# Performance work log

Measured on AMD Instinct MI355X. Metric: run time of the kernel, lower is better.

## Reference

```python
import jax, jax.numpy as jnp
import numpy as np

# DREAMPlace IDXST_IDCT (a.k.a. idsct2): y[u,v] = sum_p sum_q x[p,q] * sin(pi*p*(u+0.5)/M) * cos(pi*q*(v+0.5)/N)
# i.e. IDXST (inverse discrete sine transform, DST-III-like, unnormalized) along the M axis
# and IDCT (DCT-III-like, unnormalized, full weight on k=0) along the N axis.
# Computed with the classic 2N-padded FFT trick using the precomputed twiddles
# expk[k] = exp(-1j*pi*k/(2N)) stored as [N,2] (real, imag), matching precompute_expk.

def _idxt_spectrum(x, expk):
    """F[u] = sum_k x[k] * exp(-1j*pi*k*(2u+1)/(2N)), along last axis.
    Re(F) is the IDCT sum (cos), -Im(F) is the IDXST sum (sin)."""
    N = x.shape[-1]
    c = (x * expk[..., 0]) + 1j * (x * expk[..., 1])  # x[k] * exp(-j*pi*k/(2N))
    z = jnp.concatenate([c, jnp.zeros_like(c)], axis=-1)  # zero-pad to 2N
    return jnp.fft.fft(z, axis=-1)[..., :N]


def idct_1d(x, expk):
    # y[u] = sum_k x[k] cos(pi*k*(2u+1)/(2N))
    return _idxt_spectrum(x, expk).real


def idxst_1d(x, expk):
    # y[u] = sum_k x[k] sin(pi*k*(2u+1)/(2N))
    return -_idxt_spectrum(x, expk).imag


def _make_expk(L):
    k = jnp.arange(L, dtype=jnp.float32) * (np.pi / (2.0 * L))
    return jnp.stack([jnp.cos(k), -jnp.sin(k)], axis=-1)  # exp(-j*pi*k/(2L))


def setup_inputs() -> dict:
    M, N = 4096, 4096
    key = jax.random.key(0)
    x = jax.random.normal(key, (M, N), dtype=jnp.float32)
    return {"x": x, "expkM": _make_expk(M), "expkN": _make_expk(N)}


def reference(x, expkM, expkN):
    # IDCT along the last dim (N), then IDXST along the second-to-last dim (M):
    # idxst(idct(x)^T)^T
    t = idct_1d(x, expkN)                                        # [M, N]
    y = idxst_1d(t.swapaxes(-2, -1), expkM).swapaxes(-2, -1)     # [M, N]
    return y
```

## Files before the change

### kernel.cpp

```cpp
#include <hip/hip_runtime.h>
#include <hip/hip_bf16.h>
#include <stdint.h>
#include <cmath>


typedef __attribute__((ext_vector_type(4))) float f32x4;
typedef __attribute__((ext_vector_type(8))) unsigned short u16x8;
typedef __attribute__((ext_vector_type(8))) __bf16 bf16x8;

__device__ __forceinline__ unsigned short f2bf(float f) {
  union { float f; unsigned u; } v; v.f = f;
  unsigned u = v.u + 0x7fffu + ((v.u >> 16) & 1u);
  return (unsigned short)(u >> 16);
}
__device__ __forceinline__ float bf2f(unsigned short h) {
  union { unsigned u; float f; } v; v.u = ((unsigned)h) << 16;
  return v.f;
}

__device__ __forceinline__ void gen_half(int idx, u16x8* Pe, u16x8* Po,
                                         int isSin, int jshift, int jmask,
                                         unsigned mask4L, float sc) {
  int i = idx >> jshift;
  int jb = (idx & jmask) * 8;
  unsigned tp = 2u * (unsigned)i + 1u;
  unsigned re = (2u * (unsigned)jb * tp) & mask4L;
  unsigned ro = (re + tp) & mask4L;
  unsigned step = (2u * tp) & mask4L;
  u16x8 pe, po;
#pragma unroll
  for (int t = 0; t < 8; t++) {
    float se_, ce_, so_, co_;
    __sincosf((float)re * sc, &se_, &ce_);
    __sincosf((float)ro * sc, &so_, &co_);
    pe[t] = f2bf(isSin ? se_ : ce_);
    po[t] = f2bf(isSin ? so_ : co_);
    re = (re + step) & mask4L;
    ro = (ro + step) & mask4L;
  }
  Pe[idx] = pe;
  Po[idx] = po;
}

__global__ void prep_kernel(const f32x4* __restrict__ x, u16x8* __restrict__ xe,
                            u16x8* __restrict__ xo, u16x8* __restrict__ Ce,
                            u16x8* __restrict__ Co, u16x8* __restrict__ Se,
                            u16x8* __restrict__ So, int nConvBlocks,
                            int nGenNBlocks, int jshiftN, int jmaskN,
                            unsigned mask4N, float scN, int jshiftM, int jmaskM,
                            unsigned mask4M, float scM) {
  int b = blockIdx.x;
  if (b < nConvBlocks) {
    int idx = b * 256 + threadIdx.x;
    f32x4 a = x[4 * idx], bb = x[4 * idx + 1], c = x[4 * idx + 2],
          d = x[4 * idx + 3];
    u16x8 e, o;
    e[0] = f2bf(a[0]);  o[0] = f2bf(a[1]);  e[1] = f2bf(a[2]);  o[1] = f2bf(a[3]);
    e[2] = f2bf(bb[0]); o[2] = f2bf(bb[1]); e[3] = f2bf(bb[2]); o[3] = f2bf(bb[3]);
    e[4] = f2bf(c[0]);  o[4] = f2bf(c[1]);  e[5] = f2bf(c[2]);  o[5] = f2bf(c[3]);
    e[6] = f2bf(d[0]);  o[6] = f2bf(d[1]);  e[7] = f2bf(d[2]);  o[7] = f2bf(d[3]);
    xe[idx] = e;
    xo[idx] = o;
  } else if (b < nConvBlocks + nGenNBlocks) {
    int idx = (b - nConvBlocks) * 256 + threadIdx.x;
    gen_half(idx, Ce, Co, 0, jshiftN, jmaskN, mask4N, scN);
  } else {
    int idx = (b - nConvBlocks - nGenNBlocks) * 256 + threadIdx.x;
    gen_half(idx, Se, So, 1, jshiftM, jmaskM, mask4M, scM);
  }
}

__global__ __launch_bounds__(256, 2) void btgemm_kernel(
    const unsigned short* __restrict__ A0,
    const unsigned short* __restrict__ A1,
    const unsigned short* __restrict__ B0,
    const unsigned short* __restrict__ B1,
    unsigned short* __restrict__ C0, unsigned short* __restrict__ C1, int Ndim,
    int K) {
  __shared__ unsigned short As[128 * 64];
  __shared__ unsigned short Bs[128 * 64];

  const unsigned short* A = blockIdx.z ? A1 : A0;
  const unsigned short* Bt = blockIdx.z ? B1 : B0;
  unsigned short* C = blockIdx.z ? C1 : C0;

  const int tid = threadIdx.x;
  const int m0 = blockIdx.y * 128;
  const int n0 = blockIdx.x * 128;

  const int wave = tid >> 6;
  const int lane = tid & 63;
  const int wm = (wave & 1) * 64;
  const int wn = (wave >> 1) * 64;
  const int l16 = lane & 15;
  const int quad = lane >> 4;

  f32x4 acc[4][4];
#pragma unroll
  for (int i = 0; i < 4; i++)
#pragma unroll
    for (int j = 0; j < 4; j++) acc[i][j] = f32x4{0.f, 0.f, 0.f, 0.f};

  const int lrow = lane >> 3;
  const int lsw = ((lane & 7) ^ lrow) * 8;
  const unsigned short* Ag[4];
  const unsigned short* Bg[4];
  unsigned short* Al[4];
  unsigned short* Bl[4];
#pragma unroll
  for (int t = 0; t < 4; t++) {
    int ch = wave + 4 * t;
    Ag[t] = A + (size_t)(m0 + 8 * ch + lrow) * K + lsw;
    Bg[t] = Bt + (size_t)(n0 + 8 * ch + lrow) * K + lsw;
    Al[t] = As + ch * 512;
    Bl[t] = Bs + ch * 512;
  }

  const int swz = (quad ^ (l16 & 7)) * 8;

  for (int k0 = 0; k0 < K; k0 += 64) {
#pragma unroll
    for (int t = 0; t < 4; t++) {
      __builtin_amdgcn_global_load_lds(
          (const __attribute__((address_space(1))) void*)(Ag[t] + k0),
          (__attribute__((address_space(3))) void*)Al[t], 16, 0, 0);
      __builtin_amdgcn_global_load_lds(
          (const __attribute__((address_space(1))) void*)(Bg[t] + k0),
          (__attribute__((address_space(3))) void*)Bl[t], 16, 0, 0);
    }
    __syncthreads();

#pragma unroll
    for (int h = 0; h < 2; h++) {
      const int so = swz ^ (h * 32);
      bf16x8 af[4], bfr[4];
#pragma unroll
      for (int i = 0; i < 4; i++) {
        af[i]  = *(const bf16x8*)(As + (wm + i * 16 + l16) * 64 + so);
        bfr[i] = *(const bf16x8*)(Bs + (wn + i * 16 + l16) * 64 + so);
      }
#pragma unroll
      for (int i = 0; i < 4; i++)
#pragma unroll
        for (int j = 0; j < 4; j++)
          acc[i][j] = __builtin_amdgcn_mfma_f32_16x16x32_bf16(
              af[i], bfr[j], acc[i][j], 0, 0, 0);
    }
    __syncthreads();
  }

#pragma unroll
  for (int i = 0; i < 4; i++) {
#pragma unroll
    for (int j = 0; j < 4; j++) {
      int col = n0 + wn + j * 16 + l16;
      int rowb = m0 + wm + i * 16 + quad * 4;
#pragma unroll
      for (int r = 0; r < 4; r++)
        C[(size_t)(rowb + r) * Ndim + col] = f2bf(acc[i][j][r]);
    }
  }
}

__global__ void bfly1_kernel(const u16x8* __restrict__ E1,
                             const u16x8* __restrict__ O1,
                             u16x8* __restrict__ tTe, u16x8* __restrict__ tTo,
                             int pshift, int pmask, int Nrows, int Mh8) {
  int idx = blockIdx.x * blockDim.x + threadIdx.x;
  int v = idx >> pshift;
  int pu = idx & pmask;
  u16x8 e0 = E1[2 * idx], e1 = E1[2 * idx + 1];
  u16x8 o0 = O1[2 * idx], o1 = O1[2 * idx + 1];
  u16x8 tet, tot, teb, tob;
#pragma unroll
  for (int k = 0; k < 4; k++) {
    float ee = bf2f(e0[2 * k]), eo = bf2f(e0[2 * k + 1]);
    float oe = bf2f(o0[2 * k]), oo = bf2f(o0[2 * k + 1]);
    tet[k] = f2bf(ee + oe); tot[k] = f2bf(eo + oo);
    teb[k] = f2bf(ee - oe); tob[k] = f2bf(eo - oo);
  }
#pragma unroll
  for (int k = 0; k < 4; k++) {
    float ee = bf2f(e1[2 * k]), eo = bf2f(e1[2 * k + 1]);
    float oe = bf2f(o1[2 * k]), oo = bf2f(o1[2 * k + 1]);
    tet[4 + k] = f2bf(ee + oe); tot[4 + k] = f2bf(eo + oo);
    teb[4 + k] = f2bf(ee - oe); tob[4 + k] = f2bf(eo - oo);
  }
  tTe[idx] = tet;
  tTo[idx] = tot;
  int idxb = (Nrows - 1 - v) * Mh8 + pu;
  tTe[idxb] = teb;
  tTo[idxb] = tob;
}

__global__ void bfly2_kernel(const u16x8* __restrict__ E2,
                             const u16x8* __restrict__ O2,
                             f32x4* __restrict__ y, int vshift, int vmask,
                             int Mrows, int N4) {
  int idx = blockIdx.x * blockDim.x + threadIdx.x;
  int u = idx >> vshift;
  int vu = (idx & vmask) * 4;
  u16x8 e0 = E2[2 * idx], e1 = E2[2 * idx + 1];
  u16x8 o0 = O2[2 * idx], o1 = O2[2 * idx + 1];
  int baset = u * N4 + vu;
  int baseb = (Mrows - 1 - u) * N4 + vu;
#pragma unroll
  for (int t = 0; t < 2; t++) {
    f32x4 tv, bv;
#pragma unroll
    for (int k = 0; k < 4; k++) {
      float e = bf2f(e0[t * 4 + k]);
      float o = bf2f(o0[t * 4 + k]);
      tv[k] = e + o;
      bv[k] = o - e;
    }
    y[baset + t] = tv;
    y[baseb + t] = bv;
  }
#pragma unroll
  for (int t = 0; t < 2; t++) {
    f32x4 tv, bv;
#pragma unroll
    for (int k = 0; k < 4; k++) {
      float e = bf2f(e1[t * 4 + k]);
      float o = bf2f(o1[t * 4 + k]);
      tv[k] = e + o;
      bv[k] = o - e;
    }
    y[baset + 2 + t] = tv;
    y[baseb + 2 + t] = bv;
  }
}

extern "C" void kernel_launch(void* const* d_in, const int* in_sizes, int n_in,
                              void* d_out, int out_size, void* d_ws,
                              size_t ws_size, hipStream_t stream) {
  const float* x = (const float*)d_in[0];
  const int M = in_sizes[1] / 2;
  const int N = in_sizes[2] / 2;
  const size_t MN = (size_t)M * N;

  unsigned short* ws = (unsigned short*)d_ws;
  unsigned short* xe = ws;
  unsigned short* xo = ws + MN / 2;
  unsigned short* Ce = ws + MN;
  unsigned short* Co = ws + MN + MN / 4;
  unsigned short* Se = ws + MN * 3 / 2;
  unsigned short* So = ws + MN * 7 / 4;
  unsigned short* E1 = ws + MN * 2;
  unsigned short* O1 = ws + MN * 5 / 2;
  unsigned short* tTe = ws + MN * 3;
  unsigned short* tTo = ws + MN * 7 / 2;
  unsigned short* E2 = xe;
  unsigned short* O2 = xo;

  int shiftN = 0; while ((1 << shiftN) < N) shiftN++;
  int shiftM = 0; while ((1 << shiftM) < M) shiftM++;

  int nConvBlocks = (int)(MN / 16 / 256);
  int nGenNBlocks = (N / 2) * (N / 2) / 8 / 256;
  int nGenMBlocks = (M / 2) * (M / 2) / 8 / 256;
  prep_kernel<<<nConvBlocks + nGenNBlocks + nGenMBlocks, 256, 0, stream>>>(
      (const f32x4*)x, (u16x8*)xe, (u16x8*)xo, (u16x8*)Ce, (u16x8*)Co,
      (u16x8*)Se, (u16x8*)So, nConvBlocks, nGenNBlocks, shiftN - 4,
      (N / 16) - 1, (unsigned)(4 * N - 1),
      (float)(3.14159265358979323846 / (2.0 * N)), shiftM - 4, (M / 16) - 1,
      (unsigned)(4 * M - 1), (float)(3.14159265358979323846 / (2.0 * M)));

  btgemm_kernel<<<dim3(M / 128, (N / 2) / 128, 2), 256, 0, stream>>>(
      Ce, Co, xe, xo, E1, O1, M, N / 2);

  bfly1_kernel<<<(int)(MN / 32 / 256), 256, 0, stream>>>(
      (const u16x8*)E1, (const u16x8*)O1, (u16x8*)tTe, (u16x8*)tTo, shiftM - 4,
      (M / 16) - 1, N, M / 16);

  btgemm_kernel<<<dim3(N / 128, (M / 2) / 128, 2), 256, 0, stream>>>(
      Se, So, tTe, tTo, E2, O2, N, M / 2);

  bfly2_kernel<<<(int)(MN / 32 / 256), 256, 0, stream>>>(
      (const u16x8*)E2, (const u16x8*)O2, (f32x4*)d_out, shiftN - 4,
      (N / 16) - 1, M, N / 4);
}
```

Measured before the change: 282.3 us.

## Fuse butterfly stages into GEMM epilogues, computing even and odd products per block

Each GEMM block now computes both the even and odd partial products sequentially into two accumulator sets, then applies the butterfly (sum/difference with mirrored row) directly in the epilogue, writing either the transposed bf16 intermediate or the final fp32 output. This removes the two standalone butterfly kernels and the E/O intermediate round trips through global memory. In exchange each block does twice the K-loop work with half the grid (no z dimension), doubles accumulator registers (risking occupancy at 2 blocks/SM), and epilogue stores become scattered 2-byte/4-byte writes with strided columns.

```diff
diff --git a/kernel.cpp b/kernel.cpp
--- a/kernel.cpp
+++ b/kernel.cpp
@@ -12,10 +12,6 @@
   union { float f; unsigned u; } v; v.f = f;
   unsigned u = v.u + 0x7fffu + ((v.u >> 16) & 1u);
   return (unsigned short)(u >> 16);
-}
-__device__ __forceinline__ float bf2f(unsigned short h) {
-  union { unsigned u; float f; } v; v.u = ((unsigned)h) << 16;
-  return v.f;
 }
 
 __device__ __forceinline__ void gen_half(int idx, u16x8* Pe, u16x8* Po,
@@ -70,19 +66,16 @@
   }
 }
 
-__global__ __launch_bounds__(256, 2) void btgemm_kernel(
-    const unsigned short* __restrict__ A0,
-    const unsigned short* __restrict__ A1,
-    const unsigned short* __restrict__ B0,
-    const unsigned short* __restrict__ B1,
-    unsigned short* __restrict__ C0, unsigned short* __restrict__ C1, int Ndim,
-    int K) {
+template <int STAGE>
+__global__ __launch_bounds__(256, 2) void fused_gemm_kernel(
+    const unsigned short* __restrict__ Ae,
+    const unsigned short* __restrict__ Ao,
+    const unsigned short* __restrict__ Be,
+    const unsigned short* __restrict__ Bo,
+    unsigned short* __restrict__ out0, unsigned short* __restrict__ out1,
+    int outStride, int K, int Lfull) {
   __shared__ unsigned short As[128 * 64];
   __shared__ unsigned short Bs[128 * 64];
-
-  const unsigned short* A = blockIdx.z ? A1 : A0;
-  const unsigned short* Bt = blockIdx.z ? B1 : B0;
-  unsigned short* C = blockIdx.z ? C1 : C0;
 
   const int tid = threadIdx.x;
   const int m0 = blockIdx.y * 128;
@@ -95,140 +88,95 @@
   const int l16 = lane & 15;
   const int quad = lane >> 4;
 
-  f32x4 acc[4][4];
-#pragma unroll
-  for (int i = 0; i < 4; i++)
-#pragma unroll
-    for (int j = 0; j < 4; j++) acc[i][j] = f32x4{0.f, 0.f, 0.f, 0.f};
-
   const int lrow = lane >> 3;
   const int lsw = ((lane & 7) ^ lrow) * 8;
-  const unsigned short* Ag[4];
-  const unsigned short* Bg[4];
   unsigned short* Al[4];
   unsigned short* Bl[4];
 #pragma unroll
   for (int t = 0; t < 4; t++) {
     int ch = wave + 4 * t;
-    Ag[t] = A + (size_t)(m0 + 8 * ch + lrow) * K + lsw;
-    Bg[t] = Bt + (size_t)(n0 + 8 * ch + lrow) * K + lsw;
     Al[t] = As + ch * 512;
     Bl[t] = Bs + ch * 512;
   }
-
   const int swz = (quad ^ (l16 & 7)) * 8;
 
-  for (int k0 = 0; k0 < K; k0 += 64) {
+  f32x4 accE[4][4], accO[4][4];
+
+  auto kloop = [&](const unsigned short* __restrict__ A,
+                   const unsigned short* __restrict__ Bt,
+                   f32x4 (&acc)[4][4]) {
+#pragma unroll
+    for (int i = 0; i < 4; i++)
+#pragma unroll
+      for (int j = 0; j < 4; j++) acc[i][j] = f32x4{0.f, 0.f, 0.f, 0.f};
+
+    const unsigned short* Ag[4];
+    const unsigned short* Bg[4];
 #pragma unroll
     for (int t = 0; t < 4; t++) {
-      __builtin_amdgcn_global_load_lds(
-          (const __attribute__((address_space(1))) void*)(Ag[t] + k0),
-          (__attribute__((address_space(3))) void*)Al[t], 16, 0, 0);
-      __builtin_amdgcn_global_load_lds(
-          (const __attribute__((address_space(1))) void*)(Bg[t] + k0),
-          (__attribute__((address_space(3))) void*)Bl[t], 16, 0, 0);
+      int ch = wave + 4 * t;
+      Ag[t] = A + (size_t)(m0 + 8 * ch + lrow) * K + lsw;
+      Bg[t] = Bt + (size_t)(n0 + 8 * ch + lrow) * K + lsw;
     }
-    __syncthreads();
-
-#pragma unroll
-    for (int h = 0; h < 2; h++) {
-      const int so = swz ^ (h * 32);
-      bf16x8 af[4], bfr[4];
-#pragma unroll
-      for (int i = 0; i < 4; i++) {
-        af[i]  = *(const bf16x8*)(As + (wm + i * 16 + l16) * 64 + so);
-        bfr[i] = *(const bf16x8*)(Bs + (wn + i * 16 + l16) * 64 + so);
+
+    for (int k0 = 0; k0 < K; k0 += 64) {
+#pragma unroll
+      for (int t = 0; t < 4; t++) {
+        __builtin_amdgcn_global_load_lds(
+            (const __attribute__((address_space(1))) void*)(Ag[t] + k0),
+            (__attribute__((address_space(3))) void*)Al[t], 16, 0, 0);
+        __builtin_amdgcn_global_load_lds(
+            (const __attribute__((address_space(1))) void*)(Bg[t] + k0),
+            (__attribute__((address_space(3))) void*)Bl[t], 16, 0, 0);
       }
-#pragma unroll
-      for (int i = 0; i < 4; i++)
-#pragma unroll
-        for (int j = 0; j < 4; j++)
-          acc[i][j] = __builtin_amdgcn_mfma_f32_16x16x32_bf16(
-              af[i], bfr[j], acc[i][j], 0, 0, 0);
+      __syncthreads();
+
+#pragma unroll
+      for (int h = 0; h < 2; h++) {
+        const int so = swz ^ (h * 32);
+        bf16x8 af[4], bfr[4];
+#pragma unroll
+        for (int i = 0; i < 4; i++) {
+          af[i]  = *(const bf16x8*)(As + (wm + i * 16 + l16) * 64 + so);
+          bfr[i] = *(const bf16x8*)(Bs + (wn + i * 16 + l16) * 64 + so);
+        }
+#pragma unroll
+        for (int i = 0; i < 4; i++)
+#pragma unroll
+          for (int j = 0; j < 4; j++)
+            acc[i][j] = __builtin_amdgcn_mfma_f32_16x16x32_bf16(
+                af[i], bfr[j], acc[i][j], 0, 0, 0);
+      }
+      __syncthreads();
     }
-    __syncthreads();
-  }
+  };
+
+  kloop(Ae, Be, accE);
+  kloop(Ao, Bo, accO);
 
 #pragma unroll
   for (int i = 0; i < 4; i++) {
 #pragma unroll
     for (int j = 0; j < 4; j++) {
-      int col = n0 + wn + j * 16 + l16;
-      int rowb = m0 + wm + i * 16 + quad * 4;
-#pragma unroll
-      for (int r = 0; r < 4; r++)
-        C[(size_t)(rowb + r) * Ndim + col] = f2bf(acc[i][j][r]);
+      int n = n0 + wn + j * 16 + l16;
+      int mb = m0 + wm + i * 16 + quad * 4;
+#pragma unroll
+      for (int r = 0; r < 4; r++) {
+        float e = accE[i][j][r];
+        float o = accO[i][j][r];
+        int m = mb + r;
+        if (STAGE == 1) {
+          unsigned short* mat = (n & 1) ? out1 : out0;
+          int c = n >> 1;
+          mat[(size_t)m * outStride + c] = f2bf(e + o);
+          mat[(size_t)(Lfull - 1 - m) * outStride + c] = f2bf(e - o);
+        } else {
+          float* y = (float*)out0;
+          y[(size_t)m * outStride + n] = e + o;
+          y[(size_t)(Lfull - 1 - m) * outStride + n] = o - e;
+        }
+      }
     }
-  }
-}
-
-__global__ void bfly1_kernel(const u16x8* __restrict__ E1,
-                             const u16x8* __restrict__ O1,
-                             u16x8* __restrict__ tTe, u16x8* __restrict__ tTo,
-                             int pshift, int pmask, int Nrows, int Mh8) {
-  int idx = blockIdx.x * blockDim.x + threadIdx.x;
-  int v = idx >> pshift;
-  int pu = idx & pmask;
-  u16x8 e0 = E1[2 * idx], e1 = E1[2 * idx + 1];
-  u16x8 o0 = O1[2 * idx], o1 = O1[2 * idx + 1];
-  u16x8 tet, tot, teb, tob;
-#pragma unroll
-  for (int k = 0; k < 4; k++) {
-    float ee = bf2f(e0[2 * k]), eo = bf2f(e0[2 * k + 1]);
-    float oe = bf2f(o0[2 * k]), oo = bf2f(o0[2 * k + 1]);
-    tet[k] = f2bf(ee + oe); tot[k] = f2bf(eo + oo);
-    teb[k] = f2bf(ee - oe); tob[k] = f2bf(eo - oo);
-  }
-#pragma unroll
-  for (int k = 0; k < 4; k++) {
-    float ee = bf2f(e1[2 * k]), eo = bf2f(e1[2 * k + 1]);
-    float oe = bf2f(o1[2 * k]), oo = bf2f(o1[2 * k + 1]);
-    tet[4 + k] = f2bf(ee + oe); tot[4 + k] = f2bf(eo + oo);
-    teb[4 + k] = f2bf(ee - oe); tob[4 + k] = f2bf(eo - oo);
-  }
-  tTe[idx] = tet;
-  tTo[idx] = tot;
-  int idxb = (Nrows - 1 - v) * Mh8 + pu;
-  tTe[idxb] = teb;
-  tTo[idxb] = tob;
-}
-
-__global__ void bfly2_kernel(const u16x8* __restrict__ E2,
-                             const u16x8* __restrict__ O2,
-                             f32x4* __restrict__ y, int vshift, int vmask,
-                             int Mrows, int N4) {
-  int idx = blockIdx.x * blockDim.x + threadIdx.x;
-  int u = idx >> vshift;
-  int vu = (idx & vmask) * 4;
-  u16x8 e0 = E2[2 * idx], e1 = E2[2 * idx + 1];
-  u16x8 o0 = O2[2 * idx], o1 = O2[2 * idx + 1];
-  int baset = u * N4 + vu;
-  int baseb = (Mrows - 1 - u) * N4 + vu;
-#pragma unroll
-  for (int t = 0; t < 2; t++) {
-    f32x4 tv, bv;
-#pragma unroll
-    for (int k = 0; k < 4; k++) {
-      float e = bf2f(e0[t * 4 + k]);
-      float o = bf2f(o0[t * 4 + k]);
-      tv[k] = e + o;
-      bv[k] = o - e;
-    }
-    y[baset + t] = tv;
-    y[baseb + t] = bv;
-  }
-#pragma unroll
-  for (int t = 0; t < 2; t++) {
-    f32x4 tv, bv;
-#pragma unroll
-    for (int k = 0; k < 4; k++) {
-      float e = bf2f(e1[t * 4 + k]);
-      float o = bf2f(o1[t * 4 + k]);
-      tv[k] = e + o;
-      bv[k] = o - e;
-    }
-    y[baset + 2 + t] = tv;
-    y[baseb + 2 + t] = bv;
   }
 }
 
@@ -247,12 +195,8 @@
   unsigned short* Co = ws + MN + MN / 4;
   unsigned short* Se = ws + MN * 3 / 2;
   unsigned short* So = ws + MN * 7 / 4;
-  unsigned short* E1 = ws + MN * 2;
-  unsigned short* O1 = ws + MN * 5 / 2;
-  unsigned short* tTe = ws + MN * 3;
-  unsigned short* tTo = ws + MN * 7 / 2;
-  unsigned short* E2 = xe;
-  unsigned short* O2 = xo;
+  unsigned short* tTe = ws + MN * 2;
+  unsigned short* tTo = ws + MN * 5 / 2;
 
   int shiftN = 0; while ((1 << shiftN) < N) shiftN++;
   int shiftM = 0; while ((1 << shiftM) < M) shiftM++;
@@ -267,17 +211,9 @@
       (float)(3.14159265358979323846 / (2.0 * N)), shiftM - 4, (M / 16) - 1,
       (unsigned)(4 * M - 1), (float)(3.14159265358979323846 / (2.0 * M)));
 
-  btgemm_kernel<<<dim3(M / 128, (N / 2) / 128, 2), 256, 0, stream>>>(
-      Ce, Co, xe, xo, E1, O1, M, N / 2);
-
-  bfly1_kernel<<<(int)(MN / 32 / 256), 256, 0, stream>>>(
-      (const u16x8*)E1, (const u16x8*)O1, (u16x8*)tTe, (u16x8*)tTo, shiftM - 4,
-      (M / 16) - 1, N, M / 16);
-
-  btgemm_kernel<<<dim3(N / 128, (M / 2) / 128, 2), 256, 0, stream>>>(
-      Se, So, tTe, tTo, E2, O2, N, M / 2);
-
-  bfly2_kernel<<<(int)(MN / 32 / 256), 256, 0, stream>>>(
-      (const u16x8*)E2, (const u16x8*)O2, (f32x4*)d_out, shiftN - 4,
-      (N / 16) - 1, M, N / 4);
-}
+  fused_gemm_kernel<1><<<dim3(M / 128, (N / 2) / 128), 256, 0, stream>>>(
+      Ce, Co, xe, xo, tTe, tTo, M / 2, N / 2, N);
+
+  fused_gemm_kernel<2><<<dim3(N / 128, (M / 2) / 128), 256, 0, stream>>>(
+      Se, So, tTe, tTo, (unsigned short*)d_out, nullptr, N, M / 2, M);
+}
```

After: 272.8 us. -3.4%, faster.
